# Kernel tuning notes

Hardware: AMD Instinct MI355X
Metric: run time of the kernel (lower is better)

## Reference

```python
import jax, jax.numpy as jnp
import numpy as np

HEADS = 16
HD = 64
LN_EPS = 1e-5


def swish(x):
    return x * jax.nn.sigmoid(x)


def layer_norm(x):
    mu = jnp.mean(x, axis=-1, keepdims=True)
    var = jnp.var(x, axis=-1, keepdims=True)
    return (x - mu) * jax.lax.rsqrt(var + LN_EPS)


def setup_inputs() -> dict:
    key = jax.random.key(0)
    ks = jax.random.split(key, 5)
    B, L, D = 4, 2048, 1024
    x = jax.random.normal(ks[0], (B, L, D), dtype=jnp.float32)
    W_fc = jax.random.normal(ks[1], (D, HEADS * HD * 3), dtype=jnp.float32) * (1.0 / np.sqrt(D))
    b_fc = jax.random.normal(ks[2], (HEADS * HD * 3,), dtype=jnp.float32) * 0.01
    W_fc2 = jax.random.normal(ks[3], (HEADS * HD, D), dtype=jnp.float32) * (1.0 / np.sqrt(HEADS * HD))
    b_fc2 = jax.random.normal(ks[4], (D,), dtype=jnp.float32) * 0.01
    return {"x": x, "W_fc": W_fc, "b_fc": b_fc, "W_fc2": W_fc2, "b_fc2": b_fc2}


def reference(x, W_fc, b_fc, W_fc2, b_fc2):
    B, L, D = x.shape
    # fused QKV projection with swish activation (dropout is identity in eval)
    qkv = swish(jnp.einsum('bld,de->ble', x, W_fc) + b_fc)
    qkv = qkv.reshape(B, L, HEADS, 3 * HD)
    q, k, v = jnp.split(qkv, 3, axis=-1)  # each [B, L, H, hd]
    # NOTE: original scales by sqrt(length), not sqrt(hd)
    scores = jnp.einsum('bwhd,bmhd->bhwm', q, k) / jnp.sqrt(jnp.float32(L))
    att = jax.nn.softmax(scores, axis=-1)  # [B, H, L, L]
    new_v = jnp.einsum('bhwm,bmhd->bwhd', att, v).reshape(B, L, HEADS * HD)
    m = swish(jnp.einsum('ble,ed->bld', new_v, W_fc2) + b_fc2)
    return layer_norm(x + m)
```

## Files before the change

### kernel.cpp

```cpp
#include <hip/hip_runtime.h>
#include <cstddef>
#include <cstdint>

typedef unsigned short u16;
typedef __attribute__((ext_vector_type(8))) short short8;
typedef __attribute__((ext_vector_type(4))) float floatx4;

#define C1_SCALE 0.031882111f
#define LOG2E    1.4426950408889634f

__device__ __forceinline__ u16 f2bf(float f) {
    union { float f; unsigned int i; } v; v.f = f;
    unsigned int b = v.i;
    b += 0x7FFFu + ((b >> 16) & 1u);
    return (u16)(b >> 16);
}

__device__ __forceinline__ unsigned pk2bf(float lo, float hi) {
#if __has_builtin(__builtin_amdgcn_cvt_pk_bf16_f32)
    auto v = __builtin_amdgcn_cvt_pk_bf16_f32(lo, hi);
    union { decltype(v) b; unsigned u; } c; c.b = v; return c.u;
#else
    return (unsigned)f2bf(lo) | ((unsigned)f2bf(hi) << 16);
#endif
}
__device__ __forceinline__ int4 pack8bf(float4 a, float4 b) {
    union { unsigned u[4]; int4 v; } c;
    c.u[0] = pk2bf(a.x, a.y); c.u[1] = pk2bf(a.z, a.w);
    c.u[2] = pk2bf(b.x, b.y); c.u[3] = pk2bf(b.z, b.w);
    return c.v;
}
__device__ __forceinline__ float fastrcp(float x) {
#if __has_builtin(__builtin_amdgcn_rcpf)
    return __builtin_amdgcn_rcpf(x);
#else
    return 1.0f / x;
#endif
}
__device__ __forceinline__ float swishf(float s) {
    float e = __builtin_amdgcn_exp2f(-s * LOG2E);
    return s * fastrcp(1.0f + e);
}
__device__ __forceinline__ void glds16(const void* g, void* l) {
    __builtin_amdgcn_global_load_lds(
        (const __attribute__((address_space(1))) void*)g,
        (__attribute__((address_space(3))) void*)l, 16, 0, 0);
}

__global__ __launch_bounds__(256) void prep_kernel(
    const float* __restrict__ x,     u16* __restrict__ xb,
    const float* __restrict__ W_fc,  u16* __restrict__ WfcT,
    const float* __restrict__ W_fc2, u16* __restrict__ Wfc2T)
{
    const int id = blockIdx.x;
    if (id < 4096) {
        const size_t i = ((size_t)id * 256 + threadIdx.x) * 8;
        float4 a = *(const float4*)&x[i];
        float4 b = *(const float4*)&x[i + 4];
        *(int4*)&xb[i] = pack8bf(a, b);
        return;
    }
    __shared__ u16 t[32][33];
    const float* src; u16* dst; int R, C, bx, by;
    if (id < 7168) {
        const int w = id - 4096;
        bx = w % 96; by = w / 96; src = W_fc; dst = WfcT; R = 1024; C = 3072;
    } else {
        const int w = id - 7168;
        bx = w % 32; by = w / 32; src = W_fc2; dst = Wfc2T; R = 1024; C = 1024;
    }
    const int tx = threadIdx.x & 31, ty = threadIdx.x >> 5;
    const int r0 = by * 32, c0 = bx * 32;
#pragma unroll
    for (int i = 0; i < 4; ++i)
        t[ty + i * 8][tx] = f2bf(src[(size_t)(r0 + ty + i * 8) * C + c0 + tx]);
    __syncthreads();
#pragma unroll
    for (int i = 0; i < 4; ++i)
        dst[(size_t)(c0 + ty + i * 8) * R + r0 + tx] = t[tx][ty + i * 8];
}

#define GEMM_STAGE(AP, BP, Kdim)                                              \
    {                                                                          \
        _Pragma("unroll")                                                      \
        for (int i = 0; i < 4; ++i) {                                          \
            const int row = i * 32 + (tid >> 3);                               \
            const int gp  = (tid & 7) ^ (row & 7);                             \
            glds16(&AP[(size_t)(row0 + row) * Kdim + k0 + gp * 8],             \
                   &As[i * 32 + wid * 8][0]);                                  \
            glds16(&BP[(size_t)(col0 + row) * Kdim + k0 + gp * 8],             \
                   &Bs[i * 32 + wid * 8][0]);                                  \
        }                                                                      \
    }

#define GEMM_COMPUTE()                                                         \
    {                                                                          \
        _Pragma("unroll")                                                      \
        for (int kc = 0; kc < 2; ++kc) {                                       \
            short8 af[4], bf[4];                                               \
            const int gl = ((kc * 4 + quad) ^ (l16 & 7)) * 8;                  \
            _Pragma("unroll")                                                  \
            for (int mt = 0; mt < 4; ++mt)                                     \
                af[mt] = *(const short8*)&As[wm * 64 + mt * 16 + l16][gl];     \
            _Pragma("unroll")                                                  \
            for (int nt = 0; nt < 4; ++nt)                                     \
                bf[nt] = *(const short8*)&Bs[wn * 64 + nt * 16 + l16][gl];     \
            _Pragma("unroll")                                                  \
            for (int mt = 0; mt < 4; ++mt)                                     \
                _Pragma("unroll")                                              \
                for (int nt = 0; nt < 4; ++nt)                                 \
                    acc[mt][nt] = __builtin_amdgcn_mfma_f32_16x16x32_bf16(     \
                        af[mt], bf[nt], acc[mt][nt], 0, 0, 0);                 \
        }                                                                      \
    }

__global__ __launch_bounds__(256) void gemm_qkv_kernel(
    const u16* __restrict__ A, const u16* __restrict__ BT,
    const float* __restrict__ bias, u16* __restrict__ qk, u16* __restrict__ vT)
{
    const int K = 1024;
    const int tid  = threadIdx.x;
    const int wid  = tid >> 6;
    const int lane = tid & 63;
    const int quad = lane >> 4;
    const int l16  = lane & 15;
    const int wm = wid >> 1, wn = wid & 1;
    const int row0 = blockIdx.y * 128, col0 = blockIdx.x * 128;

    __shared__ __align__(16) u16 SMEM[2][128][64];
    auto& As = SMEM[0];
    auto& Bs = SMEM[1];
    u16 (*Vs)[136] = (u16(*)[136])&SMEM[0][0][0];

    floatx4 acc[4][4] = {};

    for (int k0 = 0; k0 < K; k0 += 64) {
        if (k0) __syncthreads();
        GEMM_STAGE(A, BT, K);
        __syncthreads();
        GEMM_COMPUTE();
    }

    float bb[4];
#pragma unroll
    for (int nt = 0; nt < 4; ++nt)
        bb[nt] = bias[col0 + wn * 64 + nt * 16 + l16];

    const int m384  = col0 % 384;
    const bool hasv = (m384 != 0);
    const int  vwn  = (m384 == 128) ? 0 : 1;
    const bool kscl = (m384 == 0 && wn == 1) || (m384 == 256 && wn == 0);
    const float scl = kscl ? C1_SCALE : 1.0f;
    const int b = row0 >> 11;

    if (hasv) __syncthreads();

#pragma unroll
    for (int mt = 0; mt < 4; ++mt) {
        const int rbase = row0 + wm * 64 + mt * 16 + quad * 4;
        const int rloc  = wm * 64 + mt * 16 + quad * 4;
#pragma unroll
        for (int nt = 0; nt < 4; ++nt) {
            float sw[4];
#pragma unroll
            for (int r = 0; r < 4; ++r)
                sw[r] = swishf(acc[mt][nt][r] + bb[nt]);
            if (hasv && wn == vwn) {
                union { u16 hh[4]; uint2 v; } pk;
#pragma unroll
                for (int r = 0; r < 4; ++r) pk.hh[r] = f2bf(sw[r]);
                *(uint2*)&Vs[nt * 16 + l16][rloc] = pk.v;
            } else {
                const int c = col0 + wn * 64 + nt * 16 + l16;
                const unsigned h = (unsigned)c / 192u;
                const int w = c - (int)h * 192;
#pragma unroll
                for (int r = 0; r < 4; ++r)
                    qk[(size_t)(rbase + r) * 2048 + h * 128 + w] = f2bf(sw[r] * scl);
            }
        }
    }

    if (hasv) {
        __syncthreads();
        const int hv = (m384 == 128) ? (col0 / 192) : ((col0 + 64) / 192);
        const int d  = tid >> 2;
        const int ch = (tid & 3) * 32;
        const int l0b = row0 & 2047;
        u16* dst = &vT[((size_t)(b * 16 + hv) * 64 + d) * 2048 + l0b + ch];
#pragma unroll
        for (int q = 0; q < 4; ++q)
            *(int4*)&dst[q * 8] = *(const int4*)&Vs[d][ch + q * 8];
    }
}

__global__ __launch_bounds__(256) void gemm_out_kernel(
    const u16* __restrict__ A, const u16* __restrict__ BT,
    const float* __restrict__ bias, const float* __restrict__ xres,
    float* __restrict__ out)
{
    const int K = 1024, N = 1024;
    const int tid  = threadIdx.x;
    const int wid  = tid >> 6;
    const int lane = tid & 63;
    const int quad = lane >> 4;
    const int l16  = lane & 15;
    const int wm = wid >> 1, wn = wid & 1;
    const int row0 = blockIdx.y * 128, col0 = blockIdx.x * 128;

    __shared__ __align__(16) u16 As[128][64];
    __shared__ __align__(16) u16 Bs[128][64];

    floatx4 acc[4][4] = {};

    for (int k0 = 0; k0 < K; k0 += 64) {
        if (k0) __syncthreads();
        GEMM_STAGE(A, BT, K);
        __syncthreads();
        GEMM_COMPUTE();
    }

    float bb[4];
#pragma unroll
    for (int nt = 0; nt < 4; ++nt)
        bb[nt] = bias[col0 + wn * 64 + nt * 16 + l16];

#pragma unroll
    for (int mt = 0; mt < 4; ++mt) {
#pragma unroll
        for (int nt = 0; nt < 4; ++nt) {
#pragma unroll
            for (int r = 0; r < 4; ++r) {
                int row = row0 + wm * 64 + mt * 16 + quad * 4 + r;
                int col = col0 + wn * 64 + nt * 16 + l16;
                float sw = swishf(acc[mt][nt][r] + bb[nt]);
                out[(size_t)row * N + col] = xres[(size_t)row * N + col] + sw;
            }
        }
    }
}

__global__ __launch_bounds__(256, 2) void attn_kernel(
    const u16* __restrict__ qk, const u16* __restrict__ vT,
    u16* __restrict__ newv)
{
    const int tid  = threadIdx.x;
    const int wid  = tid >> 6;
    const int lane = tid & 63;
    const int quad = lane >> 4;
    const int l16  = lane & 15;
    const int id = blockIdx.x;
    const int qt = id >> 6;
    const int hb = id & 63;
    const int h  = hb & 15;
    const int b  = hb >> 4;

    const u16* qkb = qk + (size_t)b * 2048 * 2048;
    const u16* vTb = vT + (size_t)(b * 16 + h) * 64 * 2048;

    short8 qf[4][2];
#pragma unroll
    for (int it = 0; it < 4; ++it) {
        const int qrow = qt * 256 + wid * 64 + it * 16 + l16;
        const u16* qp = &qkb[(size_t)qrow * 2048 + h * 128];
        qf[it][0] = *(const short8*)&qp[quad * 8];
        qf[it][1] = *(const short8*)&qp[32 + quad * 8];
    }

    const short one = (short)0x3F80;
    const short8 ones = {one, one, one, one, one, one, one, one};

    __shared__ __align__(16) u16 Ks[64][64];
    __shared__ __align__(16) u16 Vt[64][64];
    __shared__ __align__(16) u16 Ps[4][16][64];

    const int srow = tid >> 3;
    const int sg0  = (tid & 7) ^ (srow & 7);

    floatx4 oacc[4][4] = {};
    floatx4 sumacc[4] = {};

    for (int kt = 0; kt < 32; ++kt) {
        const int k0 = kt * 64;
        if (kt) __syncthreads();
#pragma unroll
        for (int i = 0; i < 2; ++i) {
            const int row = i * 32 + srow;
            glds16(&qkb[(size_t)(k0 + row) * 2048 + h * 128 + 64 + sg0 * 8],
                   &Ks[i * 32 + wid * 8][0]);
            glds16(&vTb[(size_t)row * 2048 + k0 + sg0 * 8],
                   &Vt[i * 32 + wid * 8][0]);
        }
        __syncthreads();

        short8 kf[2][4], vf[2][4];
#pragma unroll
        for (int kc = 0; kc < 2; ++kc) {
            const int gl = ((kc * 4 + quad) ^ (l16 & 7)) * 8;
#pragma unroll
            for (int nt = 0; nt < 4; ++nt) {
                kf[kc][nt] = *(const short8*)&Ks[nt * 16 + l16][gl];
                vf[kc][nt] = *(const short8*)&Vt[nt * 16 + l16][gl];
            }
        }

#pragma unroll
        for (int it = 0; it < 4; ++it) {
            floatx4 sacc[4] = {};
#pragma unroll
            for (int kc = 0; kc < 2; ++kc)
#pragma unroll
                for (int nt = 0; nt < 4; ++nt)
                    sacc[nt] = __builtin_amdgcn_mfma_f32_16x16x32_bf16(
                        kf[kc][nt], qf[it][kc], sacc[nt], 0, 0, 0);

#pragma unroll
            for (int nt = 0; nt < 4; ++nt) {
                float p0 = __builtin_amdgcn_exp2f(sacc[nt][0]);
                float p1 = __builtin_amdgcn_exp2f(sacc[nt][1]);
                float p2 = __builtin_amdgcn_exp2f(sacc[nt][2]);
                float p3 = __builtin_amdgcn_exp2f(sacc[nt][3]);
                union { unsigned u[2]; uint2 v; } pk;
                pk.u[0] = pk2bf(p0, p1);
                pk.u[1] = pk2bf(p2, p3);
                const int col = (((nt * 2 + (quad >> 1)) ^ (l16 & 7)) * 8) + (quad & 1) * 4;
                *(uint2*)&Ps[wid][l16][col] = pk.v;
            }
#pragma unroll
            for (int kc = 0; kc < 2; ++kc) {
                const int gl = ((kc * 4 + quad) ^ (l16 & 7)) * 8;
                short8 pf = *(const short8*)&Ps[wid][l16][gl];
                sumacc[it] = __builtin_amdgcn_mfma_f32_16x16x32_bf16(ones, pf, sumacc[it], 0, 0, 0);
#pragma unroll
                for (int nt = 0; nt < 4; ++nt)
                    oacc[it][nt] = __builtin_amdgcn_mfma_f32_16x16x32_bf16(
                        vf[kc][nt], pf, oacc[it][nt], 0, 0, 0);
            }
        }
    }

#pragma unroll
    for (int it = 0; it < 4; ++it) {
        const float inv = fastrcp(sumacc[it][0]);
        const int row = qt * 256 + wid * 64 + it * 16 + l16;
        u16* orow = &newv[((size_t)b * 2048 + row) * 1024 + h * 64];
#pragma unroll
        for (int nt = 0; nt < 4; ++nt) {
            union { unsigned u[2]; uint2 v; } pk;
            pk.u[0] = pk2bf(oacc[it][nt][0] * inv, oacc[it][nt][1] * inv);
            pk.u[1] = pk2bf(oacc[it][nt][2] * inv, oacc[it][nt][3] * inv);
            *(uint2*)&orow[nt * 16 + quad * 4] = pk.v;
        }
    }
}

__global__ __launch_bounds__(256) void ln_kernel(
    const float* __restrict__ y, float* __restrict__ out)
{
    const int row = blockIdx.x;
    const int tid = threadIdx.x;
    const float* yr = y + (size_t)row * 1024;
    float v[4];
    float s1 = 0.f, s2 = 0.f;
#pragma unroll
    for (int i = 0; i < 4; ++i) {
        v[i] = yr[tid + i * 256];
        s1 += v[i];
        s2 += v[i] * v[i];
    }
#pragma unroll
    for (int off = 1; off < 64; off <<= 1) {
        s1 += __shfl_xor(s1, off, 64);
        s2 += __shfl_xor(s2, off, 64);
    }
    __shared__ float red1[4], red2[4];
    const int wid = tid >> 6, lane = tid & 63;
    if (lane == 0) { red1[wid] = s1; red2[wid] = s2; }
    __syncthreads();
    s1 = red1[0] + red1[1] + red1[2] + red1[3];
    s2 = red2[0] + red2[1] + red2[2] + red2[3];
    const float mu   = s1 * (1.0f / 1024.0f);
    const float var  = s2 * (1.0f / 1024.0f) - mu * mu;
    const float rstd = rsqrtf(var + 1e-5f);
    float* orow = out + (size_t)row * 1024;
#pragma unroll
    for (int i = 0; i < 4; ++i)
        orow[tid + i * 256] = (v[i] - mu) * rstd;
}

extern "C" void kernel_launch(void* const* d_in, const int* in_sizes, int n_in,
                              void* d_out, int out_size, void* d_ws, size_t ws_size,
                              hipStream_t stream) {
    const float* x     = (const float*)d_in[0];
    const float* W_fc  = (const float*)d_in[1];
    const float* b_fc  = (const float*)d_in[2];
    const float* W_fc2 = (const float*)d_in[3];
    const float* b_fc2 = (const float*)d_in[4];
    float* out = (float*)d_out;

    char* ob = (char*)d_out;
    u16* WfcT  = (u16*)ob;
    u16* Wfc2T = (u16*)(ob + 6291456);
    u16* xbf   = (u16*)(ob + 8388608);
    u16* newv  = (u16*)(ob + 8388608);

    char* ws = (char*)d_ws;
    u16*   qk = (u16*)ws;
    u16*   vT = (u16*)(ws + 33554432);
    float* y  = (float*)ws;

    prep_kernel<<<dim3(8192), 256, 0, stream>>>(x, xbf, W_fc, WfcT, W_fc2, Wfc2T);

    gemm_qkv_kernel<<<dim3(24, 64), 256, 0, stream>>>(xbf, WfcT, b_fc, qk, vT);

    attn_kernel<<<dim3(512), 256, 0, stream>>>(qk, vT, newv);

    gemm_out_kernel<<<dim3(8, 64), 256, 0, stream>>>(newv, Wfc2T, b_fc2, x, y);

    ln_kernel<<<dim3(8192), 256, 0, stream>>>(y, out);
}
```

Before: 291.3 us.

## Split attention key range across two half-blocks and use wave-per-row layernorm

The attention kernel now runs 512 threads per block. Each half of the block processes half of the key sequence, and the partial output accumulators and row sums are combined through shared memory at the end. This doubles the waves per query tile so the 512-block grid can fill more of the GPU, at the cost of a shared-memory reduction with extra barriers. Separately, layernorm now assigns one wave per row with float4 loads and no shared-memory reduction.

```diff
diff --git a/kernel.cpp b/kernel.cpp
--- a/kernel.cpp
+++ b/kernel.cpp
@@ -240,12 +240,14 @@
     }
 }
 
-__global__ __launch_bounds__(256, 2) void attn_kernel(
+__global__ __launch_bounds__(512, 4) void attn_kernel(
     const u16* __restrict__ qk, const u16* __restrict__ vT,
     u16* __restrict__ newv)
 {
     const int tid  = threadIdx.x;
     const int wid  = tid >> 6;
+    const int half = tid >> 8;
+    const int w4   = wid & 3;
     const int lane = tid & 63;
     const int quad = lane >> 4;
     const int l16  = lane & 15;
@@ -261,7 +263,7 @@
     short8 qf[4][2];
 #pragma unroll
     for (int it = 0; it < 4; ++it) {
-        const int qrow = qt * 256 + wid * 64 + it * 16 + l16;
+        const int qrow = qt * 256 + w4 * 64 + it * 16 + l16;
         const u16* qp = &qkb[(size_t)qrow * 2048 + h * 128];
         qf[it][0] = *(const short8*)&qp[quad * 8];
         qf[it][1] = *(const short8*)&qp[32 + quad * 8];
@@ -270,26 +272,27 @@
     const short one = (short)0x3F80;
     const short8 ones = {one, one, one, one, one, one, one, one};
 
-    __shared__ __align__(16) u16 Ks[64][64];
-    __shared__ __align__(16) u16 Vt[64][64];
-    __shared__ __align__(16) u16 Ps[4][16][64];
-
-    const int srow = tid >> 3;
-    const int sg0  = (tid & 7) ^ (srow & 7);
+    __shared__ __align__(16) u16 KV[2][2][64][64];
+    __shared__ __align__(16) u16 Ps[8][16][64];
+
+    const int t256 = tid & 255;
+    const int srow = t256 >> 3;
+    const int sg0  = (t256 & 7) ^ (srow & 7);
+    const int kbase = half * 1024;
 
     floatx4 oacc[4][4] = {};
     floatx4 sumacc[4] = {};
 
-    for (int kt = 0; kt < 32; ++kt) {
-        const int k0 = kt * 64;
+    for (int kt = 0; kt < 16; ++kt) {
+        const int k0 = kbase + kt * 64;
         if (kt) __syncthreads();
 #pragma unroll
         for (int i = 0; i < 2; ++i) {
             const int row = i * 32 + srow;
             glds16(&qkb[(size_t)(k0 + row) * 2048 + h * 128 + 64 + sg0 * 8],
-                   &Ks[i * 32 + wid * 8][0]);
+                   &KV[half][0][i * 32 + w4 * 8][0]);
             glds16(&vTb[(size_t)row * 2048 + k0 + sg0 * 8],
-                   &Vt[i * 32 + wid * 8][0]);
+                   &KV[half][1][i * 32 + w4 * 8][0]);
         }
         __syncthreads();
 
@@ -299,8 +302,8 @@
             const int gl = ((kc * 4 + quad) ^ (l16 & 7)) * 8;
 #pragma unroll
             for (int nt = 0; nt < 4; ++nt) {
-                kf[kc][nt] = *(const short8*)&Ks[nt * 16 + l16][gl];
-                vf[kc][nt] = *(const short8*)&Vt[nt * 16 + l16][gl];
+                kf[kc][nt] = *(const short8*)&KV[half][0][nt * 16 + l16][gl];
+                vf[kc][nt] = *(const short8*)&KV[half][1][nt * 16 + l16][gl];
             }
         }
 
@@ -339,17 +342,32 @@
         }
     }
 
+    float* combo = (float*)&KV[0][0][0][0];
+    float* combl = (float*)&Ps[0][0][0];
 #pragma unroll
     for (int it = 0; it < 4; ++it) {
-        const float inv = fastrcp(sumacc[it][0]);
-        const int row = qt * 256 + wid * 64 + it * 16 + l16;
-        u16* orow = &newv[((size_t)b * 2048 + row) * 1024 + h * 64];
-#pragma unroll
-        for (int nt = 0; nt < 4; ++nt) {
-            union { unsigned u[2]; uint2 v; } pk;
-            pk.u[0] = pk2bf(oacc[it][nt][0] * inv, oacc[it][nt][1] * inv);
-            pk.u[1] = pk2bf(oacc[it][nt][2] * inv, oacc[it][nt][3] * inv);
-            *(uint2*)&orow[nt * 16 + quad * 4] = pk.v;
+        __syncthreads();
+        if (half == 1) {
+#pragma unroll
+            for (int nt = 0; nt < 4; ++nt)
+                *(floatx4*)&combo[(w4 * 64 + lane) * 20 + nt * 4] = oacc[it][nt];
+            combl[w4 * 64 + lane] = sumacc[it][0];
+        }
+        __syncthreads();
+        if (half == 0) {
+            const float inv = fastrcp(sumacc[it][0] + combl[w4 * 64 + lane]);
+            const int row = qt * 256 + w4 * 64 + it * 16 + l16;
+            u16* orow = &newv[((size_t)b * 2048 + row) * 1024 + h * 64];
+#pragma unroll
+            for (int nt = 0; nt < 4; ++nt) {
+                floatx4 ob = *(const floatx4*)&combo[(w4 * 64 + lane) * 20 + nt * 4];
+                union { unsigned u[2]; uint2 v; } pk;
+                pk.u[0] = pk2bf((oacc[it][nt][0] + ob[0]) * inv,
+                                (oacc[it][nt][1] + ob[1]) * inv);
+                pk.u[1] = pk2bf((oacc[it][nt][2] + ob[2]) * inv,
+                                (oacc[it][nt][3] + ob[3]) * inv);
+                *(uint2*)&orow[nt * 16 + quad * 4] = pk.v;
+            }
         }
     }
 }
@@ -357,35 +375,33 @@
 __global__ __launch_bounds__(256) void ln_kernel(
     const float* __restrict__ y, float* __restrict__ out)
 {
-    const int row = blockIdx.x;
-    const int tid = threadIdx.x;
+    const int wid = threadIdx.x >> 6, lane = threadIdx.x & 63;
+    const int row = blockIdx.x * 4 + wid;
     const float* yr = y + (size_t)row * 1024;
-    float v[4];
+    float4 v[4];
     float s1 = 0.f, s2 = 0.f;
 #pragma unroll
     for (int i = 0; i < 4; ++i) {
-        v[i] = yr[tid + i * 256];
-        s1 += v[i];
-        s2 += v[i] * v[i];
+        v[i] = *(const float4*)&yr[lane * 4 + i * 256];
+        s1 += v[i].x + v[i].y + v[i].z + v[i].w;
+        s2 += v[i].x * v[i].x + v[i].y * v[i].y + v[i].z * v[i].z + v[i].w * v[i].w;
     }
 #pragma unroll
     for (int off = 1; off < 64; off <<= 1) {
         s1 += __shfl_xor(s1, off, 64);
         s2 += __shfl_xor(s2, off, 64);
     }
-    __shared__ float red1[4], red2[4];
-    const int wid = tid >> 6, lane = tid & 63;
-    if (lane == 0) { red1[wid] = s1; red2[wid] = s2; }
-    __syncthreads();
-    s1 = red1[0] + red1[1] + red1[2] + red1[3];
-    s2 = red2[0] + red2[1] + red2[2] + red2[3];
     const float mu   = s1 * (1.0f / 1024.0f);
     const float var  = s2 * (1.0f / 1024.0f) - mu * mu;
     const float rstd = rsqrtf(var + 1e-5f);
     float* orow = out + (size_t)row * 1024;
 #pragma unroll
-    for (int i = 0; i < 4; ++i)
-        orow[tid + i * 256] = (v[i] - mu) * rstd;
+    for (int i = 0; i < 4; ++i) {
+        float4 o;
+        o.x = (v[i].x - mu) * rstd; o.y = (v[i].y - mu) * rstd;
+        o.z = (v[i].z - mu) * rstd; o.w = (v[i].w - mu) * rstd;
+        *(float4*)&orow[lane * 4 + i * 256] = o;
+    }
 }
 
 extern "C" void kernel_launch(void* const* d_in, const int* in_sizes, int n_in,
@@ -413,9 +429,9 @@
 
     gemm_qkv_kernel<<<dim3(24, 64), 256, 0, stream>>>(xbf, WfcT, b_fc, qk, vT);
 
-    attn_kernel<<<dim3(512), 256, 0, stream>>>(qk, vT, newv);
+    attn_kernel<<<dim3(512), 512, 0, stream>>>(qk, vT, newv);
 
     gemm_out_kernel<<<dim3(8, 64), 256, 0, stream>>>(newv, Wfc2T, b_fc2, x, y);
 
-    ln_kernel<<<dim3(8192), 256, 0, stream>>>(y, out);
-}
+    ln_kernel<<<dim3(2048), 256, 0, stream>>>(y, out);
+}
```

Measured after the change: 660.8 us. +126.8%, slower.

## Double-buffer K/V tiles in attention and use one wave per row in layernorm

Applied to the files above, without the earlier changes.

The attention kernel now double-buffers its K and V shared-memory tiles, issuing the async global-to-LDS loads for the next tile before computing on the current one. This removes one barrier per iteration and overlaps load latency with the MFMA work. The layernorm kernel now handles one row per wave with float4 loads and stores, which drops the LDS reduction and block barrier. Both shared buffers double in size, which may reduce occupancy.

```diff
diff --git a/kernel.cpp b/kernel.cpp
--- a/kernel.cpp
+++ b/kernel.cpp
@@ -270,8 +270,8 @@
     const short one = (short)0x3F80;
     const short8 ones = {one, one, one, one, one, one, one, one};
 
-    __shared__ __align__(16) u16 Ks[64][64];
-    __shared__ __align__(16) u16 Vt[64][64];
+    __shared__ __align__(16) u16 Ks[2][64][64];
+    __shared__ __align__(16) u16 Vt[2][64][64];
     __shared__ __align__(16) u16 Ps[4][16][64];
 
     const int srow = tid >> 3;
@@ -280,18 +280,30 @@
     floatx4 oacc[4][4] = {};
     floatx4 sumacc[4] = {};
 
+#pragma unroll
+    for (int i = 0; i < 2; ++i) {
+        const int row = i * 32 + srow;
+        glds16(&qkb[(size_t)row * 2048 + h * 128 + 64 + sg0 * 8],
+               &Ks[0][i * 32 + wid * 8][0]);
+        glds16(&vTb[(size_t)row * 2048 + sg0 * 8],
+               &Vt[0][i * 32 + wid * 8][0]);
+    }
+
     for (int kt = 0; kt < 32; ++kt) {
-        const int k0 = kt * 64;
-        if (kt) __syncthreads();
-#pragma unroll
-        for (int i = 0; i < 2; ++i) {
-            const int row = i * 32 + srow;
-            glds16(&qkb[(size_t)(k0 + row) * 2048 + h * 128 + 64 + sg0 * 8],
-                   &Ks[i * 32 + wid * 8][0]);
-            glds16(&vTb[(size_t)row * 2048 + k0 + sg0 * 8],
-                   &Vt[i * 32 + wid * 8][0]);
-        }
+        const int cur = kt & 1;
         __syncthreads();
+
+        if (kt + 1 < 32) {
+            const int k0n = (kt + 1) * 64;
+#pragma unroll
+            for (int i = 0; i < 2; ++i) {
+                const int row = i * 32 + srow;
+                glds16(&qkb[(size_t)(k0n + row) * 2048 + h * 128 + 64 + sg0 * 8],
+                       &Ks[cur ^ 1][i * 32 + wid * 8][0]);
+                glds16(&vTb[(size_t)row * 2048 + k0n + sg0 * 8],
+                       &Vt[cur ^ 1][i * 32 + wid * 8][0]);
+            }
+        }
 
         short8 kf[2][4], vf[2][4];
 #pragma unroll
@@ -299,8 +311,8 @@
             const int gl = ((kc * 4 + quad) ^ (l16 & 7)) * 8;
 #pragma unroll
             for (int nt = 0; nt < 4; ++nt) {
-                kf[kc][nt] = *(const short8*)&Ks[nt * 16 + l16][gl];
-                vf[kc][nt] = *(const short8*)&Vt[nt * 16 + l16][gl];
+                kf[kc][nt] = *(const short8*)&Ks[cur][nt * 16 + l16][gl];
+                vf[kc][nt] = *(const short8*)&Vt[cur][nt * 16 + l16][gl];
             }
         }
 
@@ -357,35 +369,33 @@
 __global__ __launch_bounds__(256) void ln_kernel(
     const float* __restrict__ y, float* __restrict__ out)
 {
-    const int row = blockIdx.x;
-    const int tid = threadIdx.x;
+    const int wid = threadIdx.x >> 6, lane = threadIdx.x & 63;
+    const int row = blockIdx.x * 4 + wid;
     const float* yr = y + (size_t)row * 1024;
-    float v[4];
+    float4 v[4];
     float s1 = 0.f, s2 = 0.f;
 #pragma unroll
     for (int i = 0; i < 4; ++i) {
-        v[i] = yr[tid + i * 256];
-        s1 += v[i];
-        s2 += v[i] * v[i];
+        v[i] = *(const float4*)&yr[lane * 4 + i * 256];
+        s1 += v[i].x + v[i].y + v[i].z + v[i].w;
+        s2 += v[i].x * v[i].x + v[i].y * v[i].y + v[i].z * v[i].z + v[i].w * v[i].w;
     }
 #pragma unroll
     for (int off = 1; off < 64; off <<= 1) {
         s1 += __shfl_xor(s1, off, 64);
         s2 += __shfl_xor(s2, off, 64);
     }
-    __shared__ float red1[4], red2[4];
-    const int wid = tid >> 6, lane = tid & 63;
-    if (lane == 0) { red1[wid] = s1; red2[wid] = s2; }
-    __syncthreads();
-    s1 = red1[0] + red1[1] + red1[2] + red1[3];
-    s2 = red2[0] + red2[1] + red2[2] + red2[3];
     const float mu   = s1 * (1.0f / 1024.0f);
     const float var  = s2 * (1.0f / 1024.0f) - mu * mu;
     const float rstd = rsqrtf(var + 1e-5f);
     float* orow = out + (size_t)row * 1024;
 #pragma unroll
-    for (int i = 0; i < 4; ++i)
-        orow[tid + i * 256] = (v[i] - mu) * rstd;
+    for (int i = 0; i < 4; ++i) {
+        float4 o;
+        o.x = (v[i].x - mu) * rstd; o.y = (v[i].y - mu) * rstd;
+        o.z = (v[i].z - mu) * rstd; o.w = (v[i].w - mu) * rstd;
+        *(float4*)&orow[lane * 4 + i * 256] = o;
+    }
 }
 
 extern "C" void kernel_launch(void* const* d_in, const int* in_sizes, int n_in,
@@ -417,5 +427,5 @@
 
     gemm_out_kernel<<<dim3(8, 64), 256, 0, stream>>>(newv, Wfc2T, b_fc2, x, y);
 
-    ln_kernel<<<dim3(8192), 256, 0, stream>>>(y, out);
-}
+    ln_kernel<<<dim3(2048), 256, 0, stream>>>(y, out);
+}
```

Result: faster. 282.6 us (-3.0%).
